# Performance work log

Hardware: AMD Instinct MI355X
Metric: run time of the kernel (lower is better)

## Reference

```python
import jax, jax.numpy as jnp
import numpy as np

B, G, N, C = 4, 64, 256, 256
HEAD = 8
HD = C // HEAD  # 32


def setup_inputs() -> dict:
    key = jax.random.key(0)
    ks = jax.random.split(key, 11)
    s = 0.02
    return {
        "q": jax.random.normal(ks[0], (B, G, N, C), jnp.float32),
        "k": jax.random.normal(ks[1], (B, G, N, C), jnp.float32),
        "v": jax.random.normal(ks[2], (B, G, N, C), jnp.float32),
        "wq": jax.random.normal(ks[3], (C, C), jnp.float32) * s,
        "bq": jnp.zeros((C,), jnp.float32),
        "wk": jax.random.normal(ks[4], (C, C), jnp.float32) * s,
        "bk": jnp.zeros((C,), jnp.float32),
        "wv": jax.random.normal(ks[5], (C, C), jnp.float32) * s,
        "bv": jnp.zeros((C,), jnp.float32),
        "wo": jax.random.normal(ks[6], (C, C), jnp.float32) * s,
        "bo": jnp.zeros((C,), jnp.float32),
    }


def reference(q, k, v, wq, bq, wk, bk, wv, bv, wo, bo):
    # Linear projections (torch Linear == x @ W.T + b; here W stored as (in,out))
    Q = q @ wq + bq  # (B,G,N,C)
    K = k @ wk + bk
    V = v @ wv + bv
    # split heads: (B,G,N,C) -> (B,G,N,H,hd)
    Qh = Q.reshape(B, G, N, HEAD, HD)
    Kh = K.reshape(B, G, N, HEAD, HD)
    Vh = V.reshape(B, G, N, HEAD, HD)
    scale = jnp.sqrt(jnp.float32(HD)) + 1e-8
    # scores: per batch b, head h, group g: (N,N)
    score = jnp.einsum("bgnhd,bgmhd->bhgnm", Qh, Kh) / scale
    attn = jax.nn.softmax(score, axis=-1)
    ctx = jnp.einsum("bhgnm,bgmhd->bgnhd", attn, Vh)  # (B,G,N,H,hd)
    ctx = ctx.reshape(B, G, N, C)
    # output projection (dropout = identity in eval)
    return ctx @ wo + bo
```

## Files before the change

### kernel.cpp

```cpp
#include <hip/hip_runtime.h>
#include <hip/hip_bf16.h>
#include <cstdint>
#include <cstddef>


typedef __attribute__((ext_vector_type(4))) float f4;
typedef __attribute__((ext_vector_type(8))) short s8;
typedef __attribute__((ext_vector_type(4))) short s4;
typedef unsigned short u16;

#define AS1 __attribute__((address_space(1)))
#define AS3 __attribute__((address_space(3)))

static constexpr int CD = 256;

__device__ __forceinline__ u16 f2bf(float f) {
    __hip_bfloat16 h = __float2bfloat16(f);
    return *reinterpret_cast<u16*>(&h);
}

__device__ __forceinline__ void gload_lds16(const void* g, void* l) {
    __builtin_amdgcn_global_load_lds((const AS1 uint32_t*)g, (AS3 uint32_t*)l, 16, 0, 0);
}

__global__ __launch_bounds__(256) void prep_k(const float* __restrict__ wq,
                                              const float* __restrict__ wk,
                                              const float* __restrict__ wv,
                                              const float* __restrict__ wo,
                                              u16* __restrict__ WT, float qs)
{
    const int bx = blockIdx.x;
    const int wsel = bx >> 4, tl = bx & 15;
    const int k0 = (tl & 3) * 64, n0 = (tl >> 2) * 64;
    const float* W = wsel == 0 ? wq : wsel == 1 ? wk : wsel == 2 ? wv : wo;
    const float scale = wsel == 0 ? qs : 1.0f;
    u16* dst = WT + (size_t)wsel * 65536;
    __shared__ float T[64][65];
    const int t = threadIdx.x;
    const int rr = t >> 4, c0 = (t & 15) * 4;
    #pragma unroll
    for (int i = 0; i < 4; ++i) {
        int r = i * 16 + rr;
        f4 f = *(const f4*)(W + (size_t)(k0 + r) * CD + n0 + c0);
        #pragma unroll
        for (int j = 0; j < 4; ++j) T[c0 + j][r] = f[j] * scale;
    }
    __syncthreads();
    #pragma unroll
    for (int i = 0; i < 4; ++i) {
        int n = i * 16 + rr;
        s4 h;
        #pragma unroll
        for (int j = 0; j < 4; ++j) h[j] = (short)f2bf(T[n][c0 + j]);
        *(s4*)(dst + (size_t)(n0 + n) * CD + k0 + c0) = h;
    }
}

template<bool A_F32, bool OUT_F32>
__device__ __forceinline__ void gemm_body(const void* __restrict__ Ain,
                                          const u16* __restrict__ Wt,
                                          const float* __restrict__ bias,
                                          float escale, void* __restrict__ Out,
                                          int d)
{
    __shared__ u16 Bs[4][64 * 64];
    const int t = threadIdx.x, lane = t & 63, w = t >> 6;
    const int n0 = ((d >> 3) & 3) * 64;
    const int m0 = (((d >> 5) << 3) | (d & 7)) * 64;
    const int lr = lane & 15, lkg = lane >> 4;
    const int lk = lkg * 8;
    const int bc = lane >> 3, bcol = (lane & 7) * 8;

    const int rowA = m0 + w * 16 + lr;

    f4 pa[16];
    s8 pb[8];
    if constexpr (A_F32) {
        const float* ap = (const float*)Ain + (size_t)rowA * CD + lk;
        #pragma unroll
        for (int ks = 0; ks < 8; ++ks) {
            pa[2 * ks]     = *(const f4*)(ap + ks * 32);
            pa[2 * ks + 1] = *(const f4*)(ap + ks * 32 + 4);
        }
    } else {
        const u16* ap = (const u16*)Ain + (size_t)rowA * CD + lk;
        #pragma unroll
        for (int ks = 0; ks < 8; ++ks)
            pb[ks] = *(const s8*)(ap + ks * 32);
    }

    #pragma unroll
    for (int ck = 0; ck < 4; ++ck) {
        #pragma unroll
        for (int j = 0; j < 2; ++j) {
            int c = j * 4 + w;
            int row = c * 8 + bc;
            int col = bcol ^ ((row & 7) << 3);
            gload_lds16(Wt + (size_t)(n0 + row) * CD + ck * 64 + col,
                        &Bs[ck][c * 512 + lane * 8]);
        }
    }
    __syncthreads();

    f4 acc[4] = {};
    #pragma unroll
    for (int ks = 0; ks < 8; ++ks) {
        s8 a;
        if constexpr (A_F32) {
            #pragma unroll
            for (int i = 0; i < 4; ++i) {
                a[i]     = (short)f2bf(pa[2 * ks][i]);
                a[i + 4] = (short)f2bf(pa[2 * ks + 1][i]);
            }
        } else {
            a = pb[ks];
        }
        const int ck = ks >> 1, kk = (ks & 1) * 32;
        #pragma unroll
        for (int n = 0; n < 4; ++n) {
            int R = n * 16 + lr;
            s8 b = *(const s8*)&Bs[ck][R * 64 + ((kk + lk) ^ ((R & 7) << 3))];
            acc[n] = __builtin_amdgcn_mfma_f32_16x16x32_bf16(a, b, acc[n], 0, 0, 0);
        }
    }

    const int orow = lkg * 4;
    #pragma unroll
    for (int n = 0; n < 4; ++n) {
        int col = n0 + n * 16 + lr;
        float bb = bias[col] * escale;
        #pragma unroll
        for (int r = 0; r < 4; ++r) {
            int row = m0 + w * 16 + orow + r;
            float vv = acc[n][r] + bb;
            if constexpr (OUT_F32)
                ((float*)Out)[(size_t)row * CD + col] = vv;
            else
                ((u16*)Out)[(size_t)row * CD + col] = f2bf(vv);
        }
    }
}

__global__ __launch_bounds__(256, 4) void gemmqkv_k(const float* q, const float* k,
        const float* v, const u16* WT, const float* bq, const float* bk,
        const float* bv, float qs, u16* Qb, u16* Kb, u16* Vb)
{
    const int op = blockIdx.x >> 12;
    const int d  = blockIdx.x & 4095;
    const float* A    = op == 0 ? q  : op == 1 ? k  : v;
    const u16*   Wt   = WT + (size_t)op * 65536;
    const float* bias = op == 0 ? bq : op == 1 ? bk : bv;
    u16*         Out  = op == 0 ? Qb : op == 1 ? Kb : Vb;
    gemm_body<true, false>(A, Wt, bias, op == 0 ? qs : 1.0f, Out, d);
}

__global__ __launch_bounds__(256, 4) void gemmo_k(const u16* Cx, const u16* WT,
                                                  const float* bo, float* out)
{
    gemm_body<false, true>(Cx, WT, bo, 1.0f, out, blockIdx.x);
}

__global__ __launch_bounds__(256, 3) void attn_k(const u16* Qb,
                                                 const u16* __restrict__ Kb,
                                                 const u16* __restrict__ Vb,
                                                 u16* Ctx)
{
    __shared__ u16 Ks[256 * 32];
    __shared__ u16 Vt[32][260];
    __shared__ u16 Ps[4][16][132];
    const int d = blockIdx.x;
    const int bg = d & 255, h = d >> 8;
    const size_t base = (size_t)bg * (256 * 256) + h * 32;
    const int t = threadIdx.x, lane = t & 63, w = t >> 6;
    const int lr = lane & 15, lk = (lane >> 4) * 8;
    const int orow = (lane >> 4) * 4;

    #pragma unroll
    for (int j = 0; j < 4; ++j) {
        int c = j * 4 + w;
        int row = c * 16 + (lane >> 2);
        int col = ((lane & 3) * 8) ^ (((row >> 1) & 3) << 3);
        gload_lds16(Kb + base + (size_t)row * CD + col, &Ks[c * 512 + lane * 8]);
    }
    {
        int n0 = (t >> 2) * 4, c0 = (t & 3) * 8;
        const u16* vp = Vb + base + (size_t)n0 * CD + c0;
        s8 r0 = *(const s8*)(vp);
        s8 r1 = *(const s8*)(vp + CD);
        s8 r2 = *(const s8*)(vp + 2 * CD);
        s8 r3 = *(const s8*)(vp + 3 * CD);
        #pragma unroll
        for (int i = 0; i < 8; ++i) {
            s4 cv = { r0[i], r1[i], r2[i], r3[i] };
            *(s4*)&Vt[c0 + i][n0] = cv;
        }
    }
    s8 aq[4];
    #pragma unroll
    for (int m = 0; m < 4; ++m)
        aq[m] = *(const s8*)(Qb + base + (size_t)(w * 64 + m * 16 + lr) * CD + lk);

    __syncthreads();

    const int myslot = lk ^ (((lr >> 1) & 3) << 3);
    const f4 zero = {0.f, 0.f, 0.f, 0.f};

    #pragma unroll
    for (int m = 0; m < 4; ++m) {
        f4 s[16];
        #pragma unroll
        for (int j = 0; j < 16; ++j) {
            s8 bk = *(const s8*)&Ks[(j * 16 + lr) * 32 + myslot];
            s[j] = __builtin_amdgcn_mfma_f32_16x16x32_bf16(aq[m], bk, zero, 0, 0, 0);
        }
        float mrow[4] = {-3.0e38f, -3.0e38f, -3.0e38f, -3.0e38f};
        #pragma unroll
        for (int j = 0; j < 16; ++j)
            #pragma unroll
            for (int r = 0; r < 4; ++r) mrow[r] = fmaxf(mrow[r], s[j][r]);
        #pragma unroll
        for (int dd = 1; dd < 16; dd <<= 1)
            #pragma unroll
            for (int r = 0; r < 4; ++r) mrow[r] = fmaxf(mrow[r], __shfl_xor(mrow[r], dd));
        float lsum[4] = {0.f, 0.f, 0.f, 0.f};
        #pragma unroll
        for (int j = 0; j < 16; ++j)
            #pragma unroll
            for (int r = 0; r < 4; ++r) {
                float p = exp2f(s[j][r] - mrow[r]);
                s[j][r] = p;
                lsum[r] += p;
            }
        #pragma unroll
        for (int dd = 1; dd < 16; dd <<= 1)
            #pragma unroll
            for (int r = 0; r < 4; ++r) lsum[r] += __shfl_xor(lsum[r], dd);

        f4 o0 = zero, o1 = zero;
        #pragma unroll
        for (int half = 0; half < 2; ++half) {
            #pragma unroll
            for (int j = 0; j < 8; ++j)
                #pragma unroll
                for (int r = 0; r < 4; ++r)
                    Ps[w][orow + r][j * 16 + lr] = f2bf(s[half * 8 + j][r]);
            #pragma unroll
            for (int kk = 0; kk < 4; ++kk) {
                s8 ap  = *(const s8*)&Ps[w][lr][kk * 32 + lk];
                s8 bv0 = *(const s8*)&Vt[lr][(half * 4 + kk) * 32 + lk];
                s8 bv1 = *(const s8*)&Vt[16 + lr][(half * 4 + kk) * 32 + lk];
                o0 = __builtin_amdgcn_mfma_f32_16x16x32_bf16(ap, bv0, o0, 0, 0, 0);
                o1 = __builtin_amdgcn_mfma_f32_16x16x32_bf16(ap, bv1, o1, 0, 0, 0);
            }
        }
        #pragma unroll
        for (int r = 0; r < 4; ++r) {
            float inv = __builtin_amdgcn_rcpf(lsum[r]);
            int row = w * 64 + m * 16 + orow + r;
            Ctx[base + (size_t)row * CD + lr]      = f2bf(o0[r] * inv);
            Ctx[base + (size_t)row * CD + 16 + lr] = f2bf(o1[r] * inv);
        }
    }
}

extern "C" void kernel_launch(void* const* d_in, const int* in_sizes, int n_in,
                              void* d_out, int out_size, void* d_ws, size_t ws_size,
                              hipStream_t stream) {
    const float* q  = (const float*)d_in[0];
    const float* k  = (const float*)d_in[1];
    const float* v  = (const float*)d_in[2];
    const float* wq = (const float*)d_in[3];
    const float* bq = (const float*)d_in[4];
    const float* wk = (const float*)d_in[5];
    const float* bk = (const float*)d_in[6];
    const float* wv = (const float*)d_in[7];
    const float* bv = (const float*)d_in[8];
    const float* wo = (const float*)d_in[9];
    const float* bo = (const float*)d_in[10];
    float* out = (float*)d_out;

    const size_t E = (size_t)65536 * 256;
    u16* Qb = (u16*)d_ws;
    u16* Kb = Qb + E;
    u16* Vb = Kb + E;
    u16* WT = Vb + E;
    u16* Cx = Qb;

    const float qs = (1.0f / (sqrtf(32.0f) + 1e-8f)) * 1.4426950408889634f;

    prep_k<<<64, 256, 0, stream>>>(wq, wk, wv, wo, WT, qs);
    gemmqkv_k<<<12288, 256, 0, stream>>>(q, k, v, WT, bq, bk, bv, qs, Qb, Kb, Vb);
    attn_k<<<2048, 256, 0, stream>>>(Qb, Kb, Vb, Cx);
    gemmo_k<<<4096, 256, 0, stream>>>(Cx, WT + 3 * 65536, bo, out);
}
```

Baseline: 227.7 us.

## Prepack weights into MFMA fragment layout and compute full-width row strips per wave

The weight prep kernel now writes each projection matrix pre-swizzled into MFMA B-fragment order, so the GEMM waves can read B fragments directly from global memory (L2-resident) with no LDS staging or block barrier. Each wave now computes a 16-row by 256-column output strip. It stages its converted A rows in a per-wave swizzled LDS strip, so each input element is read and converted exactly once instead of once per 64-column tile. Output stores become vectorized. The cost is 16 accumulator vectors per wave, which raises register pressure, and every wave repeatedly fetches the whole 128KB weight from cache.

```diff
diff --git a/kernel.cpp b/kernel.cpp
--- a/kernel.cpp
+++ b/kernel.cpp
@@ -27,137 +27,127 @@
                                               const float* __restrict__ wk,
                                               const float* __restrict__ wv,
                                               const float* __restrict__ wo,
-                                              u16* __restrict__ WT, float qs)
-{
+                                              u16* __restrict__ WTF, float qs)
+{
+    __shared__ float T[32][264];
     const int bx = blockIdx.x;
-    const int wsel = bx >> 4, tl = bx & 15;
-    const int k0 = (tl & 3) * 64, n0 = (tl >> 2) * 64;
+    const int wsel = bx >> 3, ks = bx & 7;
     const float* W = wsel == 0 ? wq : wsel == 1 ? wk : wsel == 2 ? wv : wo;
     const float scale = wsel == 0 ? qs : 1.0f;
-    u16* dst = WT + (size_t)wsel * 65536;
-    __shared__ float T[64][65];
     const int t = threadIdx.x;
-    const int rr = t >> 4, c0 = (t & 15) * 4;
-    #pragma unroll
-    for (int i = 0; i < 4; ++i) {
-        int r = i * 16 + rr;
-        f4 f = *(const f4*)(W + (size_t)(k0 + r) * CD + n0 + c0);
-        #pragma unroll
-        for (int j = 0; j < 4; ++j) T[c0 + j][r] = f[j] * scale;
+    #pragma unroll
+    for (int j = 0; j < 8; ++j) {
+        int ch = t + j * 256;
+        int row = ch >> 6, c4 = (ch & 63) * 4;
+        *(f4*)&T[row][c4] = *(const f4*)(W + (size_t)(ks * 32 + row) * CD + c4);
     }
     __syncthreads();
-    #pragma unroll
-    for (int i = 0; i < 4; ++i) {
-        int n = i * 16 + rr;
-        s4 h;
-        #pragma unroll
-        for (int j = 0; j < 4; ++j) h[j] = (short)f2bf(T[n][c0 + j]);
-        *(s4*)(dst + (size_t)(n0 + n) * CD + k0 + c0) = h;
+    u16* dst = WTF + (size_t)wsel * 65536;
+    #pragma unroll
+    for (int j = 0; j < 4; ++j) {
+        int ch = t + j * 256;
+        int lane = ch & 63, cf = ch >> 6;
+        s8 h;
+        #pragma unroll
+        for (int i = 0; i < 8; ++i)
+            h[i] = (short)f2bf(T[(lane >> 4) * 8 + i][cf * 16 + (lane & 15)] * scale);
+        *(s8*)&dst[((size_t)(ks * 16 + cf) * 64 + lane) * 8] = h;
     }
 }
 
 template<bool A_F32, bool OUT_F32>
-__device__ __forceinline__ void gemm_body(const void* __restrict__ Ain,
-                                          const u16* __restrict__ Wt,
+__device__ __forceinline__ void gemm_wave(const void* __restrict__ Ain,
+                                          const u16* __restrict__ Wf,
                                           const float* __restrict__ bias,
-                                          float escale, void* __restrict__ Out,
-                                          int d)
-{
-    __shared__ u16 Bs[4][64 * 64];
+                                          float esc, void* __restrict__ Out,
+                                          int m0, int lane, u16* S)
+{
+    const int lr = lane & 15, lg = lane >> 4;
+
+    if constexpr (A_F32) {
+        const float* A = (const float*)Ain;
+        #pragma unroll
+        for (int p = 0; p < 4; ++p) {
+            f4 r0 = *(const f4*)(A + (size_t)(m0 + p * 4 + 0) * CD + lane * 4);
+            f4 r1 = *(const f4*)(A + (size_t)(m0 + p * 4 + 1) * CD + lane * 4);
+            f4 r2 = *(const f4*)(A + (size_t)(m0 + p * 4 + 2) * CD + lane * 4);
+            f4 r3 = *(const f4*)(A + (size_t)(m0 + p * 4 + 3) * CD + lane * 4);
+            #pragma unroll
+            for (int j = 0; j < 4; ++j) {
+                f4 rr = j == 0 ? r0 : j == 1 ? r1 : j == 2 ? r2 : r3;
+                int row = p * 4 + j;
+                s4 h;
+                #pragma unroll
+                for (int i = 0; i < 4; ++i) h[i] = (short)f2bf(rr[i]);
+                *(s4*)&S[row * 256 + ((lane * 4) ^ ((row & 7) << 3))] = h;
+            }
+        }
+    } else {
+        const u16* A = (const u16*)Ain;
+        #pragma unroll
+        for (int p = 0; p < 8; ++p) {
+            int row = p * 2 + (lane >> 5);
+            int ec = (lane & 31) * 8;
+            s8 rr = *(const s8*)(A + (size_t)(m0 + row) * CD + ec);
+            *(s8*)&S[row * 256 + (ec ^ ((row & 7) << 3))] = rr;
+        }
+    }
+
+    f4 acc[16];
+    #pragma unroll
+    for (int cf = 0; cf < 16; ++cf) acc[cf] = f4{0.f, 0.f, 0.f, 0.f};
+    #pragma unroll
+    for (int ks = 0; ks < 8; ++ks) {
+        s8 af = *(const s8*)&S[lr * 256 + ((ks * 32 + lg * 8) ^ ((lr & 7) << 3))];
+        #pragma unroll
+        for (int cf = 0; cf < 16; ++cf) {
+            s8 bf = *(const s8*)(Wf + ((size_t)(ks * 16 + cf) * 64 + lane) * 8);
+            acc[cf] = __builtin_amdgcn_mfma_f32_16x16x32_bf16(bf, af, acc[cf], 0, 0, 0);
+        }
+    }
+
+    const int row = m0 + lr;
+    #pragma unroll
+    for (int cf = 0; cf < 16; ++cf) {
+        int col0 = cf * 16 + lg * 4;
+        f4 bb = *(const f4*)&bias[col0];
+        f4 vv;
+        #pragma unroll
+        for (int r = 0; r < 4; ++r) vv[r] = acc[cf][r] + bb[r] * esc;
+        if constexpr (OUT_F32) {
+            *(f4*)&((float*)Out)[(size_t)row * CD + col0] = vv;
+        } else {
+            s4 h;
+            #pragma unroll
+            for (int r = 0; r < 4; ++r) h[r] = (short)f2bf(vv[r]);
+            *(s4*)&((u16*)Out)[(size_t)row * CD + col0] = h;
+        }
+    }
+}
+
+__global__ __launch_bounds__(256, 4) void gemmqkv_k(const float* q, const float* k,
+        const float* v, const u16* WTF, const float* bq, const float* bk,
+        const float* bv, float qs, u16* Qb, u16* Kb, u16* Vb)
+{
+    __shared__ u16 strip[4][16 * 256];
     const int t = threadIdx.x, lane = t & 63, w = t >> 6;
-    const int n0 = ((d >> 3) & 3) * 64;
-    const int m0 = (((d >> 5) << 3) | (d & 7)) * 64;
-    const int lr = lane & 15, lkg = lane >> 4;
-    const int lk = lkg * 8;
-    const int bc = lane >> 3, bcol = (lane & 7) * 8;
-
-    const int rowA = m0 + w * 16 + lr;
-
-    f4 pa[16];
-    s8 pb[8];
-    if constexpr (A_F32) {
-        const float* ap = (const float*)Ain + (size_t)rowA * CD + lk;
-        #pragma unroll
-        for (int ks = 0; ks < 8; ++ks) {
-            pa[2 * ks]     = *(const f4*)(ap + ks * 32);
-            pa[2 * ks + 1] = *(const f4*)(ap + ks * 32 + 4);
-        }
-    } else {
-        const u16* ap = (const u16*)Ain + (size_t)rowA * CD + lk;
-        #pragma unroll
-        for (int ks = 0; ks < 8; ++ks)
-            pb[ks] = *(const s8*)(ap + ks * 32);
-    }
-
-    #pragma unroll
-    for (int ck = 0; ck < 4; ++ck) {
-        #pragma unroll
-        for (int j = 0; j < 2; ++j) {
-            int c = j * 4 + w;
-            int row = c * 8 + bc;
-            int col = bcol ^ ((row & 7) << 3);
-            gload_lds16(Wt + (size_t)(n0 + row) * CD + ck * 64 + col,
-                        &Bs[ck][c * 512 + lane * 8]);
-        }
-    }
-    __syncthreads();
-
-    f4 acc[4] = {};
-    #pragma unroll
-    for (int ks = 0; ks < 8; ++ks) {
-        s8 a;
-        if constexpr (A_F32) {
-            #pragma unroll
-            for (int i = 0; i < 4; ++i) {
-                a[i]     = (short)f2bf(pa[2 * ks][i]);
-                a[i + 4] = (short)f2bf(pa[2 * ks + 1][i]);
-            }
-        } else {
-            a = pb[ks];
-        }
-        const int ck = ks >> 1, kk = (ks & 1) * 32;
-        #pragma unroll
-        for (int n = 0; n < 4; ++n) {
-            int R = n * 16 + lr;
-            s8 b = *(const s8*)&Bs[ck][R * 64 + ((kk + lk) ^ ((R & 7) << 3))];
-            acc[n] = __builtin_amdgcn_mfma_f32_16x16x32_bf16(a, b, acc[n], 0, 0, 0);
-        }
-    }
-
-    const int orow = lkg * 4;
-    #pragma unroll
-    for (int n = 0; n < 4; ++n) {
-        int col = n0 + n * 16 + lr;
-        float bb = bias[col] * escale;
-        #pragma unroll
-        for (int r = 0; r < 4; ++r) {
-            int row = m0 + w * 16 + orow + r;
-            float vv = acc[n][r] + bb;
-            if constexpr (OUT_F32)
-                ((float*)Out)[(size_t)row * CD + col] = vv;
-            else
-                ((u16*)Out)[(size_t)row * CD + col] = f2bf(vv);
-        }
-    }
-}
-
-__global__ __launch_bounds__(256, 4) void gemmqkv_k(const float* q, const float* k,
-        const float* v, const u16* WT, const float* bq, const float* bk,
-        const float* bv, float qs, u16* Qb, u16* Kb, u16* Vb)
-{
-    const int op = blockIdx.x >> 12;
-    const int d  = blockIdx.x & 4095;
+    const int op = blockIdx.x >> 10;
+    const int tile = ((blockIdx.x & 1023) << 2) | w;
     const float* A    = op == 0 ? q  : op == 1 ? k  : v;
-    const u16*   Wt   = WT + (size_t)op * 65536;
+    const u16*   Wf   = WTF + (size_t)op * 65536;
     const float* bias = op == 0 ? bq : op == 1 ? bk : bv;
     u16*         Out  = op == 0 ? Qb : op == 1 ? Kb : Vb;
-    gemm_body<true, false>(A, Wt, bias, op == 0 ? qs : 1.0f, Out, d);
-}
-
-__global__ __launch_bounds__(256, 4) void gemmo_k(const u16* Cx, const u16* WT,
+    gemm_wave<true, false>(A, Wf, bias, op == 0 ? qs : 1.0f, Out,
+                           tile * 16, lane, strip[w]);
+}
+
+__global__ __launch_bounds__(256, 4) void gemmo_k(const u16* Cx, const u16* WTF,
                                                   const float* bo, float* out)
 {
-    gemm_body<false, true>(Cx, WT, bo, 1.0f, out, blockIdx.x);
+    __shared__ u16 strip[4][16 * 256];
+    const int t = threadIdx.x, lane = t & 63, w = t >> 6;
+    const int tile = (blockIdx.x << 2) | w;
+    gemm_wave<false, true>(Cx, WTF, bo, 1.0f, out, tile * 16, lane, strip[w]);
 }
 
 __global__ __launch_bounds__(256, 3) void attn_k(const u16* Qb,
@@ -283,13 +273,13 @@
     u16* Qb = (u16*)d_ws;
     u16* Kb = Qb + E;
     u16* Vb = Kb + E;
-    u16* WT = Vb + E;
+    u16* WTF = Vb + E;
     u16* Cx = Qb;
 
     const float qs = (1.0f / (sqrtf(32.0f) + 1e-8f)) * 1.4426950408889634f;
 
-    prep_k<<<64, 256, 0, stream>>>(wq, wk, wv, wo, WT, qs);
-    gemmqkv_k<<<12288, 256, 0, stream>>>(q, k, v, WT, bq, bk, bv, qs, Qb, Kb, Vb);
+    prep_k<<<32, 256, 0, stream>>>(wq, wk, wv, wo, WTF, qs);
+    gemmqkv_k<<<3072, 256, 0, stream>>>(q, k, v, WTF, bq, bk, bv, qs, Qb, Kb, Vb);
     attn_k<<<2048, 256, 0, stream>>>(Qb, Kb, Vb, Cx);
-    gemmo_k<<<4096, 256, 0, stream>>>(Cx, WT + 3 * 65536, bo, out);
-}
+    gemmo_k<<<1024, 256, 0, stream>>>(Cx, WTF + 3 * 65536, bo, out);
+}
```

New measurement: 246.6 us. 8.3% more time.
